# Kernel tuning notes

Measured on AMD Instinct MI355X. Metric: run time of the kernel, lower is better.

Reference implementation:

```python
import jax, jax.numpy as jnp
import numpy as np

N = 50000      # nodes
E = 800000     # edges
IN = 128       # in_dim
OUT = 64       # out_dim
NEG_SLOPE = 0.01  # F.leaky_relu default


def setup_inputs() -> dict:
    key = jax.random.key(0)
    k1, k2, k3, k4, k5 = jax.random.split(key, 5)
    h = jax.random.normal(k1, (N, IN), dtype=jnp.float32)
    # xavier-normal-ish scale for the two linear layers
    W_fc = jax.random.normal(k2, (OUT, IN), dtype=jnp.float32) * (2.0 / (IN + OUT)) ** 0.5
    W_attn = jax.random.normal(k3, (2 * OUT,), dtype=jnp.float32) * (2.0 / (2 * OUT + 1)) ** 0.5
    src = jax.random.randint(k4, (E,), 0, N)
    dst = jax.random.randint(k5, (E,), 0, N)
    return {"h": h, "W_fc": W_fc, "W_attn": W_attn, "src": src, "dst": dst}


def reference(h, W_fc, W_attn, src, dst):
    # z = fc(h): [N, OUT]
    z = jnp.einsum("ni,oi->no", h, W_fc)
    d = z.shape[-1]
    # per-edge attention logit: attn_fc(cat([z_src, z_dst])) == z_src@a_l + z_dst@a_r
    a_l, a_r = W_attn[:d], W_attn[d:]
    zs = z[src]                                   # [E, OUT] gather
    e = jax.nn.leaky_relu(zs @ a_l + z[dst] @ a_r, negative_slope=NEG_SLOPE)  # [E]
    # segment softmax over incoming edges of each dst node
    m = jax.ops.segment_max(e, dst, num_segments=N)          # [N]
    ex = jnp.exp(e - m[dst])                                  # [E]
    denom = jax.ops.segment_sum(ex, dst, num_segments=N)      # [N]
    alpha = ex / denom[dst]                                    # [E]
    # weighted scatter-sum of source features
    out = jax.ops.segment_sum(alpha[:, None] * zs, dst, num_segments=N)  # [N, OUT]
    return out
```

## Files before the change

### kernel.cpp

```cpp
#include <hip/hip_runtime.h>
#include <hip/hip_bf16.h>
#include <math.h>

#define IN_DIM 128
#define OUT_DIM 64
#define NEG_SLOPE 0.01f
#define BCAP 2048
#define EPT 16

typedef __attribute__((ext_vector_type(8))) short bf8_t;
typedef __attribute__((ext_vector_type(4))) float f4_t;

__device__ __forceinline__ bf8_t pack8(float4 a, float4 b) {
    union { bf8_t v; __hip_bfloat162 h[4]; } u;
    u.h[0] = __float22bfloat162_rn(make_float2(a.x, a.y));
    u.h[1] = __float22bfloat162_rn(make_float2(a.z, a.w));
    u.h[2] = __float22bfloat162_rn(make_float2(b.x, b.y));
    u.h[3] = __float22bfloat162_rn(make_float2(b.z, b.w));
    return u.v;
}

__global__ __launch_bounds__(256) void k_front(
    const int* __restrict__ src, const int* __restrict__ dst,
    int* __restrict__ bucket_cursor, unsigned* __restrict__ tmp, int E,
    const float4* __restrict__ h4, const float4* __restrict__ W4,
    const float* __restrict__ Wattn,
    __hip_bfloat16* __restrict__ zb, float* __restrict__ s_l, float* __restrict__ s_r,
    int N, int NP1)
{
    __shared__ int cntA[1024];
    __shared__ int gbase[1024];

    const int t = threadIdx.x;

    if (blockIdx.x < NP1) {
        const int base_e = blockIdx.x * (256 * EPT);

        for (int b = t; b < 1024; b += 256) cntA[b] = 0;
        __syncthreads();

        unsigned pArr[EPT];
        unsigned short rArr[EPT];
        #pragma unroll
        for (int i = 0; i < EPT; i++) {
            int ei = base_e + i * 256 + t;
            if (ei < E) {
                int s = src[ei], d = dst[ei];
                int b = d >> 6;
                pArr[i] = ((unsigned)b << 22) | ((unsigned)s << 6) | (unsigned)(d & 63);
                rArr[i] = (unsigned short)atomicAdd(&cntA[b], 1);
            } else {
                pArr[i] = 0xFFFFFFFFu;
            }
        }
        __syncthreads();

        for (int b = t; b < 1024; b += 256)
            if (cntA[b] > 0)
                gbase[b] = atomicAdd(&bucket_cursor[b], cntA[b]);
        __syncthreads();

        #pragma unroll
        for (int i = 0; i < EPT; i++) {
            unsigned p = pArr[i];
            if (p == 0xFFFFFFFFu) continue;
            int b = p >> 22;
            int slot = gbase[b] + rArr[i];
            if (slot < BCAP)
                tmp[(size_t)b * BCAP + slot] = p;
        }
    } else {
        const int lane = t & 63;
        const int wv   = t >> 6;
        const int col  = lane & 15, quad = lane >> 4;
        const int n0   = (blockIdx.x - NP1) * 64 + wv * 16;
        if (n0 >= N) return;

        bf8_t bf[4][4];
        #pragma unroll
        for (int ns = 0; ns < 4; ns++) {
            const float4* wrow = W4 + (size_t)(ns * 16 + col) * (IN_DIM / 4);
            #pragma unroll
            for (int kb = 0; kb < 4; kb++) {
                float4 x = wrow[kb * 8 + quad * 2];
                float4 y = wrow[kb * 8 + quad * 2 + 1];
                bf[kb][ns] = pack8(x, y);
            }
        }

        const int  na = n0 + col;
        const bool nv = (na < N);
        const float4* hrow = h4 + (size_t)(nv ? na : 0) * (IN_DIM / 4);
        const float4 zero = make_float4(0.f, 0.f, 0.f, 0.f);

        f4_t acc[4];
        #pragma unroll
        for (int ns = 0; ns < 4; ns++) acc[ns] = (f4_t){0.f, 0.f, 0.f, 0.f};

        #pragma unroll
        for (int kb = 0; kb < 4; kb++) {
            float4 x = nv ? hrow[kb * 8 + quad * 2]     : zero;
            float4 y = nv ? hrow[kb * 8 + quad * 2 + 1] : zero;
            bf8_t a = pack8(x, y);
            #pragma unroll
            for (int ns = 0; ns < 4; ns++)
                acc[ns] = __builtin_amdgcn_mfma_f32_16x16x32_bf16(a, bf[kb][ns], acc[ns], 0, 0, 0);
        }

        float alv[4], arv[4];
        #pragma unroll
        for (int ns = 0; ns < 4; ns++) {
            alv[ns] = Wattn[ns * 16 + col];
            arv[ns] = Wattn[OUT_DIM + ns * 16 + col];
        }
        #pragma unroll
        for (int r = 0; r < 4; r++) {
            const int nn = n0 + quad * 4 + r;
            float pl = acc[0][r] * alv[0] + acc[1][r] * alv[1] + acc[2][r] * alv[2] + acc[3][r] * alv[3];
            float pr = acc[0][r] * arv[0] + acc[1][r] * arv[1] + acc[2][r] * arv[2] + acc[3][r] * arv[3];
            #pragma unroll
            for (int o = 1; o < 16; o <<= 1) {
                pl += __shfl_xor(pl, o, 64);
                pr += __shfl_xor(pr, o, 64);
            }
            if (nn < N) {
                __hip_bfloat16* zr = zb + (size_t)nn * OUT_DIM;
                #pragma unroll
                for (int ns = 0; ns < 4; ns++)
                    zr[ns * 16 + col] = __float2bfloat16(acc[ns][r]);
                if (col == 0) { s_l[nn] = pl; s_r[nn] = pr; }
            }
        }
    }
}

__global__ __launch_bounds__(256) void k_tail(
    const unsigned* __restrict__ tmp, const int* __restrict__ bucket_cnt,
    const float* __restrict__ s_l, const float* __restrict__ s_r,
    const uint4* __restrict__ zb4, float4* __restrict__ out4, int N)
{
    __shared__ uint2 se[BCAP];
    __shared__ unsigned p2s[BCAP];
    __shared__ float exs[BCAP];
    __shared__ int cnt_s[64], off_s[64];
    __shared__ float srs[64];

    const int b = blockIdx.x, t = threadIdx.x;
    const int lane = t & 63;
    const int nbase = b * 64;
    int mb = bucket_cnt[b];
    if (mb > BCAP) mb = BCAP;

    if (t < 64) {
        cnt_s[t] = 0;
        int n = nbase + t;
        srs[t] = (n < N) ? s_r[n] : 0.f;
    }
    __syncthreads();

    const unsigned* mybuf = tmp + (size_t)b * BCAP;

    for (int i = t; i < mb; i += 256) {
        unsigned p = mybuf[i];
        int d = p & 63u;
        int s = (p >> 6) & 0xFFFFu;
        float e = s_l[s] + srs[d];
        e = (e > 0.f) ? e : NEG_SLOPE * e;
        float ex = __expf(e);
        int r = atomicAdd(&cnt_s[d], 1);
        if (r > 1023) r = 1023;
        p2s[i] = ((unsigned)r << 22) | (p & 0x3FFFFFu);
        exs[i] = ex;
    }
    __syncthreads();

    if (t < 64) {
        int c = cnt_s[t];
        int inc = c;
        #pragma unroll
        for (int o = 1; o < 64; o <<= 1) {
            int v = __shfl_up(inc, o, 64);
            if (lane >= o) inc += v;
        }
        off_s[t] = inc - c;
    }
    __syncthreads();

    for (int i = t; i < mb; i += 256) {
        unsigned q = p2s[i];
        int d = q & 63u;
        int slot = off_s[d] + (int)(q >> 22);
        if (slot < BCAP)
            se[slot] = make_uint2((q >> 6) & 0xFFFFu, __float_as_uint(exs[i]));
    }
    __syncthreads();

    const int ch8 = t & 7;
    const int grp = t >> 3;

    for (int nl = grp; nl < 64; nl += 32) {
        const int n = nbase + nl;
        if (n >= N) continue;
        const int beg = off_s[nl];
        int end = beg + cnt_s[nl];
        if (end > BCAP) end = BCAP;
        float4* op = out4 + (size_t)n * 16 + ch8 * 2;

        if (end <= beg) {
            op[0] = make_float4(0.f, 0.f, 0.f, 0.f);
            op[1] = make_float4(0.f, 0.f, 0.f, 0.f);
            continue;
        }

        float a0 = 0.f, a1 = 0.f, a2 = 0.f, a3 = 0.f;
        float a4 = 0.f, a5 = 0.f, a6 = 0.f, a7 = 0.f;
        float dsum = 0.f;

        #pragma unroll 4
        for (int i = beg; i < end; ++i) {
            uint2 q = se[i];
            float ex = __uint_as_float(q.y);
            dsum += ex;
            uint4 zv = zb4[(size_t)q.x * 8 + ch8];
            float f0 = __uint_as_float(zv.x << 16);
            float f1 = __uint_as_float(zv.x & 0xffff0000u);
            float f2 = __uint_as_float(zv.y << 16);
            float f3 = __uint_as_float(zv.y & 0xffff0000u);
            float f4 = __uint_as_float(zv.z << 16);
            float f5 = __uint_as_float(zv.z & 0xffff0000u);
            float f6 = __uint_as_float(zv.w << 16);
            float f7 = __uint_as_float(zv.w & 0xffff0000u);
            a0 += ex * f0; a1 += ex * f1; a2 += ex * f2; a3 += ex * f3;
            a4 += ex * f4; a5 += ex * f5; a6 += ex * f6; a7 += ex * f7;
        }

        float inv = 1.f / dsum;
        op[0] = make_float4(a0 * inv, a1 * inv, a2 * inv, a3 * inv);
        op[1] = make_float4(a4 * inv, a5 * inv, a6 * inv, a7 * inv);
    }
}

extern "C" void kernel_launch(void* const* d_in, const int* in_sizes, int n_in,
                              void* d_out, int out_size, void* d_ws, size_t ws_size,
                              hipStream_t stream)
{
    const float* h     = (const float*)d_in[0];
    const float* Wfc   = (const float*)d_in[1];
    const float* Wattn = (const float*)d_in[2];
    const int*   src   = (const int*)d_in[3];
    const int*   dst   = (const int*)d_in[4];
    const int N = in_sizes[0] / IN_DIM;
    const int E = in_sizes[3];
    const int NBK = (N + 63) / 64;
    const int NP1 = (E + 256 * EPT - 1) / (256 * EPT);

    __hip_bfloat16* zb = (__hip_bfloat16*)d_ws;
    float* s_l     = (float*)(zb + (size_t)N * OUT_DIM);
    float* s_r     = s_l + N;
    int*   bcursor = (int*)(s_r + N);
    unsigned* tmp  = (unsigned*)(bcursor + 1024);

    const int nblk_g = (N + 63) / 64;

    hipMemsetAsync(bcursor, 0, 1024 * sizeof(int), stream);

    k_front<<<NP1 + nblk_g, 256, 0, stream>>>(src, dst, bcursor, tmp, E,
                                              (const float4*)h, (const float4*)Wfc, Wattn,
                                              zb, s_l, s_r, N, NP1);
    k_tail <<<NBK, 256, 0, stream>>>(tmp, bcursor, s_l, s_r,
                                     (const uint4*)zb, (float4*)d_out, N);
}
```

Baseline: 133.0 us.

## Fuse front and tail into one persistent kernel with a grid barrier

Merges the bucketing/GEMM kernel and the per-bucket softmax-aggregate kernel into a single persistent kernel. Blocks loop over work items and meet at an atomic-counter grid barrier, removing one kernel launch and the gap between them. Shared memory is overlaid through a union, and BCAP is reduced to 1792 to shrink the tail's LDS footprint and raise occupancy. The fused path depends on every block being co-resident to avoid deadlock, hardcodes 256 CUs in the capacity estimate, and a smaller BCAP raises the risk of dropping edges in high-degree buckets.

```diff
diff --git a/kernel.cpp b/kernel.cpp
--- a/kernel.cpp
+++ b/kernel.cpp
@@ -5,11 +5,16 @@
 #define IN_DIM 128
 #define OUT_DIM 64
 #define NEG_SLOPE 0.01f
-#define BCAP 2048
+#define BCAP 1792
 #define EPT 16
 
 typedef __attribute__((ext_vector_type(8))) short bf8_t;
 typedef __attribute__((ext_vector_type(4))) float f4_t;
+
+struct FrontSm { int cntA[1024]; int gbase[1024]; };
+struct TailSm  { uint2 se[BCAP]; unsigned p2s[BCAP]; float exs[BCAP];
+                 int cnt_s[64]; int off_s[64]; float srs[64]; };
+union SmU { FrontSm f; TailSm t; };
 
 __device__ __forceinline__ bf8_t pack8(float4 a, float4 b) {
     union { bf8_t v; __hip_bfloat162 h[4]; } u;
@@ -20,141 +25,132 @@
     return u.v;
 }
 
-__global__ __launch_bounds__(256) void k_front(
+__device__ void part1_body(int bid, int t,
     const int* __restrict__ src, const int* __restrict__ dst,
     int* __restrict__ bucket_cursor, unsigned* __restrict__ tmp, int E,
+    int* cntA, int* gbase)
+{
+    const int base_e = bid * (256 * EPT);
+
+    for (int b = t; b < 1024; b += 256) cntA[b] = 0;
+    __syncthreads();
+
+    unsigned pArr[EPT];
+    unsigned short rArr[EPT];
+    #pragma unroll
+    for (int i = 0; i < EPT; i++) {
+        int ei = base_e + i * 256 + t;
+        if (ei < E) {
+            int s = src[ei], d = dst[ei];
+            int b = d >> 6;
+            pArr[i] = ((unsigned)b << 22) | ((unsigned)s << 6) | (unsigned)(d & 63);
+            rArr[i] = (unsigned short)atomicAdd(&cntA[b], 1);
+        } else {
+            pArr[i] = 0xFFFFFFFFu;
+        }
+    }
+    __syncthreads();
+
+    for (int b = t; b < 1024; b += 256)
+        if (cntA[b] > 0)
+            gbase[b] = atomicAdd(&bucket_cursor[b], cntA[b]);
+    __syncthreads();
+
+    #pragma unroll
+    for (int i = 0; i < EPT; i++) {
+        unsigned p = pArr[i];
+        if (p == 0xFFFFFFFFu) continue;
+        int b = p >> 22;
+        int slot = gbase[b] + rArr[i];
+        if (slot < BCAP)
+            tmp[(size_t)b * BCAP + slot] = p;
+    }
+}
+
+__device__ void gemm_body(int gb, int t,
     const float4* __restrict__ h4, const float4* __restrict__ W4,
     const float* __restrict__ Wattn,
     __hip_bfloat16* __restrict__ zb, float* __restrict__ s_l, float* __restrict__ s_r,
-    int N, int NP1)
-{
-    __shared__ int cntA[1024];
-    __shared__ int gbase[1024];
-
-    const int t = threadIdx.x;
-
-    if (blockIdx.x < NP1) {
-        const int base_e = blockIdx.x * (256 * EPT);
-
-        for (int b = t; b < 1024; b += 256) cntA[b] = 0;
-        __syncthreads();
-
-        unsigned pArr[EPT];
-        unsigned short rArr[EPT];
-        #pragma unroll
-        for (int i = 0; i < EPT; i++) {
-            int ei = base_e + i * 256 + t;
-            if (ei < E) {
-                int s = src[ei], d = dst[ei];
-                int b = d >> 6;
-                pArr[i] = ((unsigned)b << 22) | ((unsigned)s << 6) | (unsigned)(d & 63);
-                rArr[i] = (unsigned short)atomicAdd(&cntA[b], 1);
-            } else {
-                pArr[i] = 0xFFFFFFFFu;
-            }
-        }
-        __syncthreads();
-
-        for (int b = t; b < 1024; b += 256)
-            if (cntA[b] > 0)
-                gbase[b] = atomicAdd(&bucket_cursor[b], cntA[b]);
-        __syncthreads();
-
-        #pragma unroll
-        for (int i = 0; i < EPT; i++) {
-            unsigned p = pArr[i];
-            if (p == 0xFFFFFFFFu) continue;
-            int b = p >> 22;
-            int slot = gbase[b] + rArr[i];
-            if (slot < BCAP)
-                tmp[(size_t)b * BCAP + slot] = p;
-        }
-    } else {
-        const int lane = t & 63;
-        const int wv   = t >> 6;
-        const int col  = lane & 15, quad = lane >> 4;
-        const int n0   = (blockIdx.x - NP1) * 64 + wv * 16;
-        if (n0 >= N) return;
-
-        bf8_t bf[4][4];
-        #pragma unroll
-        for (int ns = 0; ns < 4; ns++) {
-            const float4* wrow = W4 + (size_t)(ns * 16 + col) * (IN_DIM / 4);
-            #pragma unroll
-            for (int kb = 0; kb < 4; kb++) {
-                float4 x = wrow[kb * 8 + quad * 2];
-                float4 y = wrow[kb * 8 + quad * 2 + 1];
-                bf[kb][ns] = pack8(x, y);
-            }
-        }
-
-        const int  na = n0 + col;
-        const bool nv = (na < N);
-        const float4* hrow = h4 + (size_t)(nv ? na : 0) * (IN_DIM / 4);
-        const float4 zero = make_float4(0.f, 0.f, 0.f, 0.f);
-
-        f4_t acc[4];
-        #pragma unroll
-        for (int ns = 0; ns < 4; ns++) acc[ns] = (f4_t){0.f, 0.f, 0.f, 0.f};
-
+    int N)
+{
+    const int lane = t & 63;
+    const int wv   = t >> 6;
+    const int col  = lane & 15, quad = lane >> 4;
+    const int n0   = gb * 64 + wv * 16;
+    if (n0 >= N) return;
+
+    bf8_t bf[4][4];
+    #pragma unroll
+    for (int ns = 0; ns < 4; ns++) {
+        const float4* wrow = W4 + (size_t)(ns * 16 + col) * (IN_DIM / 4);
         #pragma unroll
         for (int kb = 0; kb < 4; kb++) {
-            float4 x = nv ? hrow[kb * 8 + quad * 2]     : zero;
-            float4 y = nv ? hrow[kb * 8 + quad * 2 + 1] : zero;
-            bf8_t a = pack8(x, y);
+            float4 x = wrow[kb * 8 + quad * 2];
+            float4 y = wrow[kb * 8 + quad * 2 + 1];
+            bf[kb][ns] = pack8(x, y);
+        }
+    }
+
+    const int  na = n0 + col;
+    const bool nv = (na < N);
+    const float4* hrow = h4 + (size_t)(nv ? na : 0) * (IN_DIM / 4);
+    const float4 zero = make_float4(0.f, 0.f, 0.f, 0.f);
+
+    f4_t acc[4];
+    #pragma unroll
+    for (int ns = 0; ns < 4; ns++) acc[ns] = (f4_t){0.f, 0.f, 0.f, 0.f};
+
+    #pragma unroll
+    for (int kb = 0; kb < 4; kb++) {
+        float4 x = nv ? hrow[kb * 8 + quad * 2]     : zero;
+        float4 y = nv ? hrow[kb * 8 + quad * 2 + 1] : zero;
+        bf8_t a = pack8(x, y);
+        #pragma unroll
+        for (int ns = 0; ns < 4; ns++)
+            acc[ns] = __builtin_amdgcn_mfma_f32_16x16x32_bf16(a, bf[kb][ns], acc[ns], 0, 0, 0);
+    }
+
+    float alv[4], arv[4];
+    #pragma unroll
+    for (int ns = 0; ns < 4; ns++) {
+        alv[ns] = Wattn[ns * 16 + col];
+        arv[ns] = Wattn[OUT_DIM + ns * 16 + col];
+    }
+    #pragma unroll
+    for (int r = 0; r < 4; r++) {
+        const int nn = n0 + quad * 4 + r;
+        float pl = acc[0][r] * alv[0] + acc[1][r] * alv[1] + acc[2][r] * alv[2] + acc[3][r] * alv[3];
+        float pr = acc[0][r] * arv[0] + acc[1][r] * arv[1] + acc[2][r] * arv[2] + acc[3][r] * arv[3];
+        #pragma unroll
+        for (int o = 1; o < 16; o <<= 1) {
+            pl += __shfl_xor(pl, o, 64);
+            pr += __shfl_xor(pr, o, 64);
+        }
+        if (nn < N) {
+            __hip_bfloat16* zr = zb + (size_t)nn * OUT_DIM;
             #pragma unroll
             for (int ns = 0; ns < 4; ns++)
-                acc[ns] = __builtin_amdgcn_mfma_f32_16x16x32_bf16(a, bf[kb][ns], acc[ns], 0, 0, 0);
-        }
-
-        float alv[4], arv[4];
-        #pragma unroll
-        for (int ns = 0; ns < 4; ns++) {
-            alv[ns] = Wattn[ns * 16 + col];
-            arv[ns] = Wattn[OUT_DIM + ns * 16 + col];
-        }
-        #pragma unroll
-        for (int r = 0; r < 4; r++) {
-            const int nn = n0 + quad * 4 + r;
-            float pl = acc[0][r] * alv[0] + acc[1][r] * alv[1] + acc[2][r] * alv[2] + acc[3][r] * alv[3];
-            float pr = acc[0][r] * arv[0] + acc[1][r] * arv[1] + acc[2][r] * arv[2] + acc[3][r] * arv[3];
-            #pragma unroll
-            for (int o = 1; o < 16; o <<= 1) {
-                pl += __shfl_xor(pl, o, 64);
-                pr += __shfl_xor(pr, o, 64);
-            }
-            if (nn < N) {
-                __hip_bfloat16* zr = zb + (size_t)nn * OUT_DIM;
-                #pragma unroll
-                for (int ns = 0; ns < 4; ns++)
-                    zr[ns * 16 + col] = __float2bfloat16(acc[ns][r]);
-                if (col == 0) { s_l[nn] = pl; s_r[nn] = pr; }
-            }
-        }
-    }
-}
-
-__global__ __launch_bounds__(256) void k_tail(
+                zr[ns * 16 + col] = __float2bfloat16(acc[ns][r]);
+            if (col == 0) { s_l[nn] = pl; s_r[nn] = pr; }
+        }
+    }
+}
+
+__device__ void tail_body(int b, int t,
     const unsigned* __restrict__ tmp, const int* __restrict__ bucket_cnt,
     const float* __restrict__ s_l, const float* __restrict__ s_r,
-    const uint4* __restrict__ zb4, float4* __restrict__ out4, int N)
-{
-    __shared__ uint2 se[BCAP];
-    __shared__ unsigned p2s[BCAP];
-    __shared__ float exs[BCAP];
-    __shared__ int cnt_s[64], off_s[64];
-    __shared__ float srs[64];
-
-    const int b = blockIdx.x, t = threadIdx.x;
+    const uint4* __restrict__ zb4, float4* __restrict__ out4, int N,
+    TailSm* sm)
+{
     const int lane = t & 63;
     const int nbase = b * 64;
     int mb = bucket_cnt[b];
     if (mb > BCAP) mb = BCAP;
 
     if (t < 64) {
-        cnt_s[t] = 0;
+        sm->cnt_s[t] = 0;
         int n = nbase + t;
-        srs[t] = (n < N) ? s_r[n] : 0.f;
+        sm->srs[t] = (n < N) ? s_r[n] : 0.f;
     }
     __syncthreads();
 
@@ -164,34 +160,34 @@
         unsigned p = mybuf[i];
         int d = p & 63u;
         int s = (p >> 6) & 0xFFFFu;
-        float e = s_l[s] + srs[d];
+        float e = s_l[s] + sm->srs[d];
         e = (e > 0.f) ? e : NEG_SLOPE * e;
         float ex = __expf(e);
-        int r = atomicAdd(&cnt_s[d], 1);
+        int r = atomicAdd(&sm->cnt_s[d], 1);
         if (r > 1023) r = 1023;
-        p2s[i] = ((unsigned)r << 22) | (p & 0x3FFFFFu);
-        exs[i] = ex;
+        sm->p2s[i] = ((unsigned)r << 22) | (p & 0x3FFFFFu);
+        sm->exs[i] = ex;
     }
     __syncthreads();
 
     if (t < 64) {
-        int c = cnt_s[t];
+        int c = sm->cnt_s[t];
         int inc = c;
         #pragma unroll
         for (int o = 1; o < 64; o <<= 1) {
             int v = __shfl_up(inc, o, 64);
             if (lane >= o) inc += v;
         }
-        off_s[t] = inc - c;
+        sm->off_s[t] = inc - c;
     }
     __syncthreads();
 
     for (int i = t; i < mb; i += 256) {
-        unsigned q = p2s[i];
+        unsigned q = sm->p2s[i];
         int d = q & 63u;
-        int slot = off_s[d] + (int)(q >> 22);
+        int slot = sm->off_s[d] + (int)(q >> 22);
         if (slot < BCAP)
-            se[slot] = make_uint2((q >> 6) & 0xFFFFu, __float_as_uint(exs[i]));
+            sm->se[slot] = make_uint2((q >> 6) & 0xFFFFu, __float_as_uint(sm->exs[i]));
     }
     __syncthreads();
 
@@ -201,8 +197,8 @@
     for (int nl = grp; nl < 64; nl += 32) {
         const int n = nbase + nl;
         if (n >= N) continue;
-        const int beg = off_s[nl];
-        int end = beg + cnt_s[nl];
+        const int beg = sm->off_s[nl];
+        int end = beg + sm->cnt_s[nl];
         if (end > BCAP) end = BCAP;
         float4* op = out4 + (size_t)n * 16 + ch8 * 2;
 
@@ -218,7 +214,7 @@
 
         #pragma unroll 4
         for (int i = beg; i < end; ++i) {
-            uint2 q = se[i];
+            uint2 q = sm->se[i];
             float ex = __uint_as_float(q.y);
             dsum += ex;
             uint4 zv = zb4[(size_t)q.x * 8 + ch8];
@@ -240,6 +236,72 @@
     }
 }
 
+__device__ __forceinline__ void grid_barrier(int* bar, int nblk)
+{
+    __syncthreads();
+    if (threadIdx.x == 0) {
+        __threadfence();
+        atomicAdd(bar, 1);
+        while (__hip_atomic_load(bar, __ATOMIC_RELAXED, __HIP_MEMORY_SCOPE_AGENT) < nblk)
+            __builtin_amdgcn_s_sleep(2);
+        __threadfence();
+    }
+    __syncthreads();
+}
+
+__global__ __launch_bounds__(256) void k_fused(
+    const int* __restrict__ src, const int* __restrict__ dst,
+    int* __restrict__ bucket_cursor, int* __restrict__ bar,
+    unsigned* __restrict__ tmp, int E,
+    const float4* __restrict__ h4, const float4* __restrict__ W4,
+    const float* __restrict__ Wattn,
+    __hip_bfloat16* __restrict__ zb, float* __restrict__ s_l, float* __restrict__ s_r,
+    float4* __restrict__ out4, int N, int NP1, int NG, int NBK)
+{
+    __shared__ SmU sm;
+    const int t = threadIdx.x;
+
+    for (int bid = blockIdx.x; bid < NP1 + NG; bid += gridDim.x) {
+        if (bid < NP1)
+            part1_body(bid, t, src, dst, bucket_cursor, tmp, E, sm.f.cntA, sm.f.gbase);
+        else
+            gemm_body(bid - NP1, t, h4, W4, Wattn, zb, s_l, s_r, N);
+        __syncthreads();
+    }
+
+    grid_barrier(bar, (int)gridDim.x);
+
+    for (int bid = blockIdx.x; bid < NBK; bid += gridDim.x) {
+        tail_body(bid, t, tmp, bucket_cursor, s_l, s_r, (const uint4*)zb, out4, N, &sm.t);
+        __syncthreads();
+    }
+}
+
+__global__ __launch_bounds__(256) void k_front(
+    const int* __restrict__ src, const int* __restrict__ dst,
+    int* __restrict__ bucket_cursor, unsigned* __restrict__ tmp, int E,
+    const float4* __restrict__ h4, const float4* __restrict__ W4,
+    const float* __restrict__ Wattn,
+    __hip_bfloat16* __restrict__ zb, float* __restrict__ s_l, float* __restrict__ s_r,
+    int N, int NP1)
+{
+    __shared__ FrontSm sm;
+    const int t = threadIdx.x;
+    if ((int)blockIdx.x < NP1)
+        part1_body(blockIdx.x, t, src, dst, bucket_cursor, tmp, E, sm.cntA, sm.gbase);
+    else
+        gemm_body(blockIdx.x - NP1, t, h4, W4, Wattn, zb, s_l, s_r, N);
+}
+
+__global__ __launch_bounds__(256) void k_tail(
+    const unsigned* __restrict__ tmp, const int* __restrict__ bucket_cnt,
+    const float* __restrict__ s_l, const float* __restrict__ s_r,
+    const uint4* __restrict__ zb4, float4* __restrict__ out4, int N)
+{
+    __shared__ TailSm sm;
+    tail_body(blockIdx.x, threadIdx.x, tmp, bucket_cnt, s_l, s_r, zb4, out4, N, &sm);
+}
+
 extern "C" void kernel_launch(void* const* d_in, const int* in_sizes, int n_in,
                               void* d_out, int out_size, void* d_ws, size_t ws_size,
                               hipStream_t stream)
@@ -253,20 +315,36 @@
     const int E = in_sizes[3];
     const int NBK = (N + 63) / 64;
     const int NP1 = (E + 256 * EPT - 1) / (256 * EPT);
+    const int NG  = (N + 63) / 64;
+    const int TOTAL = NP1 + NG;
 
     __hip_bfloat16* zb = (__hip_bfloat16*)d_ws;
     float* s_l     = (float*)(zb + (size_t)N * OUT_DIM);
     float* s_r     = s_l + N;
     int*   bcursor = (int*)(s_r + N);
-    unsigned* tmp  = (unsigned*)(bcursor + 1024);
-
-    const int nblk_g = (N + 63) / 64;
-
-    hipMemsetAsync(bcursor, 0, 1024 * sizeof(int), stream);
-
-    k_front<<<NP1 + nblk_g, 256, 0, stream>>>(src, dst, bcursor, tmp, E,
-                                              (const float4*)h, (const float4*)Wfc, Wattn,
-                                              zb, s_l, s_r, N, NP1);
-    k_tail <<<NBK, 256, 0, stream>>>(tmp, bcursor, s_l, s_r,
-                                     (const uint4*)zb, (float4*)d_out, N);
-}
+    int*   bar     = bcursor + 1024;
+    unsigned* tmp  = (unsigned*)(bcursor + 1040);
+
+    hipMemsetAsync(bcursor, 0, 1040 * sizeof(int), stream);
+
+    static int s_blocks_per_cu = -2;
+    if (s_blocks_per_cu == -2) {
+        int nb = 0;
+        hipError_t e = hipOccupancyMaxActiveBlocksPerMultiprocessor(&nb, k_fused, 256, 0);
+        s_blocks_per_cu = (e == hipSuccess && nb > 0) ? nb : 0;
+    }
+    const int capacity = s_blocks_per_cu * 256;
+
+    if (capacity >= 512) {
+        const int GRID = (TOTAL < capacity) ? TOTAL : capacity;
+        k_fused<<<GRID, 256, 0, stream>>>(src, dst, bcursor, bar, tmp, E,
+                                          (const float4*)h, (const float4*)Wfc, Wattn,
+                                          zb, s_l, s_r, (float4*)d_out, N, NP1, NG, NBK);
+    } else {
+        k_front<<<TOTAL, 256, 0, stream>>>(src, dst, bcursor, tmp, E,
+                                           (const float4*)h, (const float4*)Wfc, Wattn,
+                                           zb, s_l, s_r, N, NP1);
+        k_tail <<<NBK, 256, 0, stream>>>(tmp, bcursor, s_l, s_r,
+                                         (const uint4*)zb, (float4*)d_out, N);
+    }
+}
```

New measurement: 145.8 us. 1.1x slower.
